# Kernel tuning notes

Measured on AMD Instinct MI355X. Metric: run time of the kernel, lower is better.

The kernel has to match this reference:

```python
import jax, jax.numpy as jnp
import numpy as np


def _quantum_act(x, act_w):
    # LearnedQuantumActivation, eval mode (no phase noise): softmax-weighted mix of 9 activations
    w = jax.nn.softmax(act_w)
    mish = x * jnp.tanh(jax.nn.softplus(x))
    return (w[0] * jax.nn.sigmoid(x) + w[1] * jax.nn.elu(x) + w[2] * jnp.tanh(x)
            + w[3] * jax.nn.relu(x) + w[4] * jax.nn.silu(x)
            + w[5] * jax.nn.gelu(x, approximate=False) + w[6] * jax.nn.selu(x)
            + w[7] * mish + w[8] * x)


def setup_inputs() -> dict:
    B, D, U, N = 1024, 1024, 2048, 4      # batch, input_dim, max_units, num_branches
    M, MD, O, H = 2048, 1024, 512, 64     # memory_size, memory_dim, output_dim, critic hidden
    key = jax.random.key(0)
    ks = jax.random.split(key, 16)
    g = lambda k, shape, s=0.02: jax.random.normal(k, shape, dtype=jnp.float32) * s
    return {
        "x": jax.random.normal(ks[0], (B, D), dtype=jnp.float32),
        "w": g(ks[1], (D, U, N)),
        "b": jnp.zeros((U, N), jnp.float32),
        "gate_w": g(ks[2], (D, N)), "gate_b": jnp.zeros((N,), jnp.float32),
        "act_w": jnp.ones((9,), jnp.float32),
        "mask": jnp.ones((U,), jnp.float32),          # neuron_mask, initial_units == max_units
        "mem": g(ks[3], (M, MD), 0.05),
        "att_w": g(ks[4], (U, M)), "att_b": jnp.zeros((M,), jnp.float32),
        "write_w": g(ks[5], (U, MD)), "write_b": jnp.zeros((MD,), jnp.float32),
        "update_gate": jnp.full((M,), 0.5, jnp.float32),
        "out_w": g(ks[6], (U, O)), "out_b": jnp.zeros((O,), jnp.float32),
        "cw1": g(ks[7], (MD, H // 2)), "cb1": jnp.zeros((H // 2,), jnp.float32),
        "cw2": g(ks[8], (O, H // 2)), "cb2": jnp.zeros((H // 2,), jnp.float32),
        "cw3": g(ks[9], (U, H // 2)), "cb3": jnp.zeros((H // 2,), jnp.float32),
        "cw4": g(ks[10], (3 * (H // 2), H)), "cb4": jnp.zeros((H,), jnp.float32),
        "cw5": g(ks[11], (H, 2)), "cb5": jnp.zeros((2,), jnp.float32),
        "meta_threshold": jnp.float32(0.5),
    }


def reference(x, w, b, gate_w, gate_b, act_w, mask, mem, att_w, att_b,
              write_w, write_b, update_gate, out_w, out_b,
              cw1, cb1, cw2, cb2, cw3, cb3, cw4, cb4, cw5, cb5, meta_threshold):
    # Dendritic plastic dense: per-branch projections mixed by a learned softmax branch gate
    pre = jnp.einsum('bi,iun->bun', x, w) + b               # (B, U, N)
    gate = jax.nn.softmax(x @ gate_w + gate_b, axis=-1)     # (B, N)
    hidden = _quantum_act(jnp.einsum('bun,bn->bu', pre, gate), act_w) * mask  # (B, U)
    # Episodic memory read + write (write is returned instead of in-place assign)
    read_att = jax.nn.softmax(hidden @ att_w + att_b, axis=-1)  # (B, M)
    read = read_att @ mem                                       # (B, MD)
    cand = jnp.tanh(hidden @ write_w + write_b)                 # (B, MD)
    u = (jnp.mean(read_att, axis=0) * update_gate)[:, None]     # (M, 1)
    new_mem = mem * (1.0 - u) + u * jnp.mean(cand, axis=0)      # (M, MD)
    # Prediction head
    preds = hidden @ out_w + out_b                              # (B, O)
    # Metacognitive critic gating
    mf = jax.nn.relu(read @ cw1 + cb1)
    pf = jax.nn.relu(preds @ cw2 + cb2)
    hf = jax.nn.relu(hidden @ cw3 + cb3)
    fused = jax.nn.relu(jnp.concatenate([mf, pf, hf], axis=-1) @ cw4 + cb4)
    outs = fused @ cw5 + cb5
    gating = jax.nn.sigmoid(outs[:, 0:1] - meta_threshold)
    return (preds * gating, new_mem)
```

## Files before the change

kernel.cpp:

```cpp
#include <hip/hip_runtime.h>
#include <hip/hip_bf16.h>
#include <math.h>

typedef __attribute__((ext_vector_type(4))) float f32x4;
typedef __attribute__((ext_vector_type(8))) short s16x8;
typedef __attribute__((ext_vector_type(4))) short s16x4;
typedef __hip_bfloat16 bf16;

#define MB (1024ull*1024ull)
#define GATE_OFF    (0ull)
#define ACTW_OFF    (16ull*1024)
#define U_OFF       (20ull*1024)
#define CMEAN_OFF   (28ull*1024)
#define PART_OFF    (64ull*1024)
#define HIDDEN_OFF  (1ull*MB)
#define RATT_OFF    (5ull*MB)
#define CAND_OFF    (9ull*MB)
#define PREDS_OFF   (11ull*MB)
#define READ_OFF    (13ull*MB)
#define XBF_OFF     (17ull*MB)
#define WT_OFF      (19ull*MB)
#define CATT_OFF    (35ull*MB)
#define MEMT_OFF    (49ull*MB)
#define READ2_OFF   WT_OFF

__device__ __forceinline__ short f2bf_s(float f) {
    bf16 h = __float2bfloat16(f);
    return *reinterpret_cast<short*>(&h);
}

__device__ __forceinline__ void async_load16(const bf16* g, short* l) {
    __builtin_amdgcn_global_load_lds((const __attribute__((address_space(1))) void*)g,
                                     (__attribute__((address_space(3))) void*)l, 16, 0, 0);
}

__device__ __forceinline__ float fast_tanh(float x) {
    float e2x = __expf(2.f * x);
    return 1.f - 2.f / (e2x + 1.f);
}

__device__ __forceinline__ float qact(float x, const float* w) {
    float ex  = __expf(x);
    float r1  = 1.f / (1.f + ex);
    float sig = 1.f - r1;
    float em1 = ex - 1.f;
    float elu = x > 0.f ? x : em1;
    float e2x = ex * ex;
    float th  = 1.f - 2.f / (e2x + 1.f);
    float rel = fmaxf(x, 0.f);
    float silu = x * sig;
    float u   = 0.7978845608028654f * (x + 0.044715f * x * x * x);
    float e2u = __expf(2.f * u);
    float gel = x * (1.f - 1.f / (e2u + 1.f));
    float sel = 1.0507009873554805f * (x > 0.f ? x : 1.6732632423543772f * em1);
    float t   = 1.f + ex;
    float t2  = t * t;
    float mish = x * (1.f - 2.f / (t2 + 1.f));
    return w[0]*sig + w[1]*elu + w[2]*th + w[3]*rel + w[4]*silu
         + w[5]*gel + w[6]*sel + w[7]*mish + w[8]*x;
}

__device__ __forceinline__ void do_transpose(const float* __restrict__ in,
                                             bf16* __restrict__ out, int R, int C,
                                             int bx, int by, int t) {
    __shared__ short tile[64][66];
    int k0 = by*64, n0 = bx*64;
    int tx = t & 63, ty = t >> 6;
    #pragma unroll
    for (int j = 0; j < 16; j++) {
        int k = ty + j*4;
        tile[tx][k] = f2bf_s(in[(size_t)(k0 + k)*C + n0 + tx]);
    }
    __syncthreads();
    int kp = t & 31, nrow = t >> 5;
    #pragma unroll
    for (int jj = 0; jj < 8; jj++) {
        int n = nrow + jj*8;
        unsigned lo = (unsigned short)tile[n][kp*2];
        unsigned hi = (unsigned short)tile[n][kp*2 + 1];
        *reinterpret_cast<unsigned*>(&out[(size_t)(n0 + n)*R + k0 + kp*2]) = lo | (hi << 16);
    }
}

__global__ __launch_bounds__(256) void k_prepass(
        const float* __restrict__ x, bf16* __restrict__ xbf,
        const float* __restrict__ gw, const float* __restrict__ gb,
        const float* __restrict__ aw_in,
        float* __restrict__ gate, float* __restrict__ actw,
        const float* __restrict__ w_, bf16* __restrict__ wT,
        const float* __restrict__ att_w, const float* __restrict__ write_w,
        const float* __restrict__ out_w, bf16* __restrict__ catT,
        const float* __restrict__ mem, bf16* __restrict__ memT) {
    int blk = blockIdx.x, t = threadIdx.x;
    if (blk < 1024) {
        int i = blk*256 + t;
        f32x4 v = ((const f32x4*)x)[i];
        s16x4 o;
        #pragma unroll
        for (int j = 0; j < 4; j++) o[j] = f2bf_s(v[j]);
        ((s16x4*)xbf)[i] = o;
        if (blk == 0 && t == 64) {
            float a[9]; float m = -1e30f;
            for (int i2 = 0; i2 < 9; i2++) { a[i2] = aw_in[i2]; m = fmaxf(m, a[i2]); }
            float ss = 0.f;
            for (int i2 = 0; i2 < 9; i2++) { a[i2] = __expf(a[i2]-m); ss += a[i2]; }
            float inv = 1.f / ss;
            for (int i2 = 0; i2 < 9; i2++) actw[i2] = a[i2]*inv;
        }
    } else if (blk < 2048) {
        int b = blk - 1024, w = t >> 6, lane = t & 63;
        __shared__ float l[4];
        float s = 0.f;
        for (int k = lane; k < 1024; k += 64)
            s += x[(size_t)b*1024 + k] * gw[k*4 + w];
        #pragma unroll
        for (int off = 32; off; off >>= 1) s += __shfl_xor(s, off);
        if (lane == 0) l[w] = s + gb[w];
        __syncthreads();
        if (t == 0) {
            float m = fmaxf(fmaxf(l[0], l[1]), fmaxf(l[2], l[3]));
            float e0 = __expf(l[0]-m), e1 = __expf(l[1]-m), e2 = __expf(l[2]-m), e3 = __expf(l[3]-m);
            float inv = 1.f / (e0+e1+e2+e3);
            gate[b*4+0] = e0*inv; gate[b*4+1] = e1*inv;
            gate[b*4+2] = e2*inv; gate[b*4+3] = e3*inv;
        }
    } else if (blk < 4096) {
        int rel = blk - 2048;
        do_transpose(w_, wT, 1024, 8192, rel & 127, rel >> 7, t);
    } else if (blk < 5120) {
        int rel = blk - 4096;
        do_transpose(att_w, catT, 2048, 2048, rel & 31, rel >> 5, t);
    } else if (blk < 5632) {
        int rel = blk - 5120;
        do_transpose(write_w, catT + 2048ull*2048, 2048, 1024, rel & 15, rel >> 4, t);
    } else if (blk < 5888) {
        int rel = blk - 5632;
        do_transpose(out_w, catT + 3072ull*2048, 2048, 512, rel & 7, rel >> 3, t);
    } else {
        int rel = blk - 5888;
        do_transpose(mem, memT, 2048, 1024, rel & 15, rel >> 4, t);
    }
}

template <int MODE, int TM>
__global__ __launch_bounds__(256, 2) void gemm_bt(
        const bf16* __restrict__ A, const bf16* __restrict__ Bt,
        int K, int lda, int ldb, int kOffset,
        const float* __restrict__ bias, const float* __restrict__ bias2,
        const float* __restrict__ bias3,
        float* __restrict__ outF, float* __restrict__ outF2,
        bf16* __restrict__ outH, bf16* __restrict__ outH2,
        const float* __restrict__ gate, const float* __restrict__ actw,
        const float* __restrict__ mask, int outStride) {
    constexpr int MI = TM / 32;
    __shared__ __align__(16) union SMem {
        struct { short a[2][TM*32]; short b[2][128*32]; } tl;
        float z[TM*32];
    } sm;
    int t = threadIdx.x, lane = t & 63;
    int rowBase = blockIdx.y * TM, colBase = blockIdx.x * 128;
    int lm = lane & 15, lq = lane >> 4;
    int w = t >> 6;
    int qm = (w >> 1) * (TM/2), qn = (w & 1) * 64;

    A  += (size_t)kOffset * blockIdx.z;
    Bt += (size_t)kOffset * blockIdx.z;

    f32x4 acc[MI][4];
    #pragma unroll
    for (int i = 0; i < MI; i++)
        #pragma unroll
        for (int j = 0; j < 4; j++) acc[i][j] = (f32x4){0.f, 0.f, 0.f, 0.f};

    int cb0 = w*128 + lane, cb1 = cb0 + 64;
    int rb0 = cb0 >> 2, kb0 = (cb0 & 3) * 8;
    int rb1 = cb1 >> 2, kb1 = (cb1 & 3) * 8;
    int ca0 = (TM == 128) ? (w*128 + lane) : (w*64 + lane);
    int ra0 = ca0 >> 2, ka0 = (ca0 & 3) * 8;
    int ra1 = (ca0 + 64) >> 2, ka1 = ((ca0 + 64) & 3) * 8;

    auto issueLoads = [&](int k0, int ib) {
        short* bA = sm.tl.a[ib];
        short* bB = sm.tl.b[ib];
        async_load16(A + (size_t)(rowBase + ra0)*lda + k0 + ka0,
                     bA + ((TM == 128) ? w*1024 : w*512));
        if (TM == 128)
            async_load16(A + (size_t)(rowBase + ra1)*lda + k0 + ka1, bA + w*1024 + 512);
        async_load16(Bt + (size_t)(colBase + rb0)*ldb + k0 + kb0, bB + w*1024);
        async_load16(Bt + (size_t)(colBase + rb1)*ldb + k0 + kb1, bB + w*1024 + 512);
    };

    issueLoads(0, 0);
    int ib = 0;
    for (int k0 = 0; k0 < K; k0 += 32) {
        __syncthreads();
        if (k0 + 32 < K) issueLoads(k0 + 32, ib ^ 1);
        const short* cA = sm.tl.a[ib];
        const short* cB = sm.tl.b[ib];
        s16x8 af[MI], bfr[4];
        #pragma unroll
        for (int mi = 0; mi < MI; mi++)
            af[mi] = *reinterpret_cast<const s16x8*>(cA + (qm + mi*16 + lm)*32 + lq*8);
        #pragma unroll
        for (int ni = 0; ni < 4; ni++)
            bfr[ni] = *reinterpret_cast<const s16x8*>(cB + (qn + ni*16 + lm)*32 + lq*8);
        #pragma unroll
        for (int mi = 0; mi < MI; mi++)
            #pragma unroll
            for (int ni = 0; ni < 4; ni++)
                acc[mi][ni] = __builtin_amdgcn_mfma_f32_16x16x32_bf16(af[mi], bfr[ni], acc[mi][ni], 0, 0, 0);
        ib ^= 1;
    }

    if (MODE == 4) {
        __syncthreads();
        #pragma unroll
        for (int mi = 0; mi < MI; mi++) {
            int rowl0 = qm + mi*16 + lq*4;
            #pragma unroll
            for (int ni = 0; ni < 4; ni++) {
                int col = colBase + qn + ni*16 + lm;
                int n = col & 3;
                float bb = bias[col];
                f32x4 v = acc[mi][ni];
                #pragma unroll
                for (int r = 0; r < 4; r++) v[r] = (v[r] + bb) * gate[(rowBase + rowl0 + r)*4 + n];
                #pragma unroll
                for (int r = 0; r < 4; r++) v[r] += __shfl_xor(v[r], 1);
                #pragma unroll
                for (int r = 0; r < 4; r++) v[r] += __shfl_xor(v[r], 2);
                if ((lane & 3) == 0) {
                    int ul = ((w & 1) << 4) + ni*4 + (lm >> 2);
                    #pragma unroll
                    for (int r = 0; r < 4; r++)
                        sm.z[(rowl0 + r)*32 + ul] = v[r];
                }
            }
        }
        __syncthreads();
        float aw[9];
        #pragma unroll
        for (int i = 0; i < 9; i++) aw[i] = actw[i];
        int u0 = colBase >> 2;
        #pragma unroll
        for (int i = 0; i < TM/8; i++) {
            int idx = t + i*256;
            int row = idx >> 5, ul = idx & 31;
            int ug = u0 + ul;
            float zz = sm.z[idx];
            outH[(size_t)(rowBase + row)*outStride + ug] = __float2bfloat16(qact(zz, aw) * mask[ug]);
        }
    } else if (MODE == 5) {
        #pragma unroll
        for (int mi = 0; mi < MI; mi++) {
            int row0 = rowBase + qm + mi*16 + lq*4;
            #pragma unroll
            for (int ni = 0; ni < 4; ni++) {
                int col = colBase + qn + ni*16 + lm;
                if (col < 2048) {
                    float bb = bias[col];
                    #pragma unroll
                    for (int r = 0; r < 4; r++)
                        outH[(size_t)(row0 + r)*2048 + col] = __float2bfloat16(acc[mi][ni][r] + bb);
                } else if (col < 3072) {
                    int c = col - 2048;
                    float bb = bias2[c];
                    #pragma unroll
                    for (int r = 0; r < 4; r++)
                        outH2[(size_t)(row0 + r)*1024 + c] = __float2bfloat16(fast_tanh(acc[mi][ni][r] + bb));
                } else {
                    int c = col - 3072;
                    float bb = bias3[c];
                    #pragma unroll
                    for (int r = 0; r < 4; r++)
                        outF[(size_t)(row0 + r)*512 + c] = acc[mi][ni][r] + bb;
                }
            }
        }
    } else {
        float* of = blockIdx.z ? outF2 : outF;
        #pragma unroll
        for (int mi = 0; mi < MI; mi++) {
            int row0 = rowBase + qm + mi*16 + lq*4;
            #pragma unroll
            for (int ni = 0; ni < 4; ni++) {
                int col = colBase + qn + ni*16 + lm;
                #pragma unroll
                for (int r = 0; r < 4; r++)
                    of[(size_t)(row0 + r)*outStride + col] = acc[mi][ni][r];
            }
        }
    }
}

__global__ __launch_bounds__(256) void k_softmax(bf16* __restrict__ ratt) {
    int b = blockIdx.x, t = threadIdx.x, w = t >> 6, lane = t & 63;
    __shared__ float red[8];
    bf16* row = ratt + (size_t)b*2048;
    float v[8];
    float mx = -1e30f;
    #pragma unroll
    for (int j = 0; j < 8; j++) {
        v[j] = __bfloat162float(row[t + j*256]);
        mx = fmaxf(mx, v[j]);
    }
    #pragma unroll
    for (int off = 32; off; off >>= 1) mx = fmaxf(mx, __shfl_xor(mx, off));
    if (lane == 0) red[w] = mx;
    __syncthreads();
    mx = fmaxf(fmaxf(red[0], red[1]), fmaxf(red[2], red[3]));
    float s = 0.f;
    #pragma unroll
    for (int j = 0; j < 8; j++) { v[j] = __expf(v[j] - mx); s += v[j]; }
    #pragma unroll
    for (int off = 32; off; off >>= 1) s += __shfl_xor(s, off);
    if (lane == 0) red[4 + w] = s;
    __syncthreads();
    float inv = 1.f / (red[4] + red[5] + red[6] + red[7]);
    #pragma unroll
    for (int j = 0; j < 8; j++)
        row[t + j*256] = __float2bfloat16(v[j] * inv);
}

__global__ __launch_bounds__(256) void k_colpart(const bf16* __restrict__ ratt,
                                                 const bf16* __restrict__ cand,
                                                 float* __restrict__ part) {
    int ct = blockIdx.x, rc = blockIdx.y, t = threadIdx.x;
    int col = ct*256 + t;
    const bf16* src; int stride, c;
    if (ct < 8) { src = ratt; stride = 2048; c = col; }
    else        { src = cand; stride = 1024; c = col - 2048; }
    float s = 0.f;
    int r0 = rc*128;
    for (int r = 0; r < 128; r++)
        s += __bfloat162float(src[(size_t)(r0 + r)*stride + c]);
    part[rc*3072 + col] = s;
}

__global__ __launch_bounds__(256) void k_colfin(const float* __restrict__ part,
                                                const float* __restrict__ update_gate,
                                                float* __restrict__ u,
                                                float* __restrict__ cmean) {
    int col = blockIdx.x*256 + threadIdx.x;
    float s = 0.f;
    #pragma unroll
    for (int rc = 0; rc < 8; rc++) s += part[rc*3072 + col];
    s *= (1.f/1024.f);
    if (col < 2048) u[col] = s * update_gate[col];
    else            cmean[col - 2048] = s;
}

__global__ __launch_bounds__(256) void k_newmem(const float* __restrict__ mem,
                                                const float* __restrict__ u,
                                                const float* __restrict__ cmean,
                                                float* __restrict__ out1) {
    int idx = blockIdx.x*256 + threadIdx.x;
    int m = idx >> 10, d = idx & 1023;
    float um = u[m];
    out1[idx] = mem[idx] * (1.f - um) + um * cmean[d];
}

__global__ __launch_bounds__(256) void k_critic(
        const float* __restrict__ readv, const float* __restrict__ readv2,
        const float* __restrict__ preds, const bf16* __restrict__ hidden,
        const float* cw1, const float* cb1, const float* cw2, const float* cb2,
        const float* cw3, const float* cb3, const float* cw4, const float* cb4,
        const float* cw5, const float* cb5, const float* thr,
        float* __restrict__ out0) {
    __shared__ __align__(16) float sx[2*1024];
    __shared__ __align__(16) float sp[2*512];
    __shared__ __align__(16) short sh[2*2048];
    __shared__ __align__(16) f32x4 part[2][32][8];
    __shared__ float feat[2][96];
    __shared__ float fused[2][64];
    __shared__ float gsh[2];
    int b0 = blockIdx.x * 2, t = threadIdx.x;
    int j4 = t & 7, kg = t >> 3;

    ((f32x4*)sx)[t]       = ((const f32x4*)(readv + (size_t)b0*1024))[t]
                          + ((const f32x4*)(readv2 + (size_t)b0*1024))[t];
    ((f32x4*)sx)[t + 256] = ((const f32x4*)(readv + (size_t)b0*1024))[t + 256]
                          + ((const f32x4*)(readv2 + (size_t)b0*1024))[t + 256];
    ((f32x4*)sp)[t]       = ((const f32x4*)(preds + (size_t)b0*512))[t];
    ((s16x8*)sh)[t]       = ((const s16x8*)(hidden + (size_t)b0*2048))[t];
    ((s16x8*)sh)[t + 256] = ((const s16x8*)(hidden + (size_t)b0*2048))[t + 256];
    __syncthreads();

    {
        const f32x4* wv = (const f32x4*)cw1;
        f32x4 a0 = (f32x4){0,0,0,0}, a1 = (f32x4){0,0,0,0};
        int k0 = kg*32;
        #pragma unroll 4
        for (int k = k0; k < k0 + 32; k++) {
            f32x4 wq = wv[k*8 + j4];
            a0 += sx[k] * wq;
            a1 += sx[1024 + k] * wq;
        }
        part[0][kg][j4] = a0; part[1][kg][j4] = a1;
    }
    __syncthreads();
    if (t < 64) {
        int r = t >> 5, f = t & 31;
        float s = 0.f;
        #pragma unroll
        for (int i = 0; i < 32; i++) s += part[r][i][f >> 2][f & 3];
        feat[r][f] = fmaxf(s + cb1[f], 0.f);
    }
    __syncthreads();
    {
        const f32x4* wv = (const f32x4*)cw2;
        f32x4 a0 = (f32x4){0,0,0,0}, a1 = (f32x4){0,0,0,0};
        int k0 = kg*16;
        #pragma unroll 4
        for (int k = k0; k < k0 + 16; k++) {
            f32x4 wq = wv[k*8 + j4];
            a0 += sp[k] * wq;
            a1 += sp[512 + k] * wq;
        }
        part[0][kg][j4] = a0; part[1][kg][j4] = a1;
    }
    __syncthreads();
    if (t < 64) {
        int r = t >> 5, f = t & 31;
        float s = 0.f;
        #pragma unroll
        for (int i = 0; i < 32; i++) s += part[r][i][f >> 2][f & 3];
        feat[r][32 + f] = fmaxf(s + cb2[f], 0.f);
    }
    __syncthreads();
    {
        const f32x4* wv = (const f32x4*)cw3;
        f32x4 a0 = (f32x4){0,0,0,0}, a1 = (f32x4){0,0,0,0};
        int k0 = kg*64;
        #pragma unroll 4
        for (int k = k0; k < k0 + 64; k++) {
            f32x4 wq = wv[k*8 + j4];
            float h0 = __bfloat162float(*reinterpret_cast<const bf16*>(&sh[k]));
            float h1 = __bfloat162float(*reinterpret_cast<const bf16*>(&sh[2048 + k]));
            a0 += h0 * wq;
            a1 += h1 * wq;
        }
        part[0][kg][j4] = a0; part[1][kg][j4] = a1;
    }
    __syncthreads();
    if (t < 64) {
        int r = t >> 5, f = t & 31;
        float s = 0.f;
        #pragma unroll
        for (int i = 0; i < 32; i++) s += part[r][i][f >> 2][f & 3];
        feat[r][64 + f] = fmaxf(s + cb3[f], 0.f);
    }
    __syncthreads();
    if (t < 128) {
        int r = t >> 6, uu = t & 63;
        float s = 0.f;
        #pragma unroll 8
        for (int k = 0; k < 96; k++) s += feat[r][k] * cw4[k*64 + uu];
        fused[r][uu] = fmaxf(s + cb4[uu], 0.f);
    }
    __syncthreads();
    if (t < 128) {
        int r = t >> 6, lane = t & 63;
        float v = fused[r][lane] * cw5[lane*2];
        #pragma unroll
        for (int off = 32; off; off >>= 1) v += __shfl_xor(v, off);
        if (lane == 0)
            gsh[r] = 1.f / (1.f + __expf(-(v + cb5[0] - thr[0])));
    }
    __syncthreads();
    #pragma unroll
    for (int idx = t; idx < 1024; idx += 256) {
        int r = idx >> 9, o = idx & 511;
        out0[(size_t)(b0 + r)*512 + o] = sp[r*512 + o] * gsh[r];
    }
}

extern "C" void kernel_launch(void* const* d_in, const int* in_sizes, int n_in,
                              void* d_out, int out_size, void* d_ws, size_t ws_size,
                              hipStream_t stream) {
    const float* x        = (const float*)d_in[0];
    const float* w_       = (const float*)d_in[1];
    const float* b_bias   = (const float*)d_in[2];
    const float* gate_w   = (const float*)d_in[3];
    const float* gate_b   = (const float*)d_in[4];
    const float* act_w    = (const float*)d_in[5];
    const float* mask     = (const float*)d_in[6];
    const float* mem      = (const float*)d_in[7];
    const float* att_w    = (const float*)d_in[8];
    const float* att_b    = (const float*)d_in[9];
    const float* write_w  = (const float*)d_in[10];
    const float* write_b  = (const float*)d_in[11];
    const float* upd_gate = (const float*)d_in[12];
    const float* out_w    = (const float*)d_in[13];
    const float* out_b    = (const float*)d_in[14];
    const float* cw1 = (const float*)d_in[15]; const float* cb1 = (const float*)d_in[16];
    const float* cw2 = (const float*)d_in[17]; const float* cb2 = (const float*)d_in[18];
    const float* cw3 = (const float*)d_in[19]; const float* cb3 = (const float*)d_in[20];
    const float* cw4 = (const float*)d_in[21]; const float* cb4 = (const float*)d_in[22];
    const float* cw5 = (const float*)d_in[23]; const float* cb5 = (const float*)d_in[24];
    const float* thr = (const float*)d_in[25];

    char* ws = (char*)d_ws;
    float* gate   = (float*)(ws + GATE_OFF);
    float* actw   = (float*)(ws + ACTW_OFF);
    float* uvec   = (float*)(ws + U_OFF);
    float* cmean  = (float*)(ws + CMEAN_OFF);
    float* part   = (float*)(ws + PART_OFF);
    bf16*  hidden = (bf16*)(ws + HIDDEN_OFF);
    bf16*  ratt   = (bf16*)(ws + RATT_OFF);
    bf16*  cand   = (bf16*)(ws + CAND_OFF);
    float* preds  = (float*)(ws + PREDS_OFF);
    float* readv  = (float*)(ws + READ_OFF);
    float* readv2 = (float*)(ws + READ2_OFF);
    bf16*  xbf    = (bf16*)(ws + XBF_OFF);
    bf16*  wT     = (bf16*)(ws + WT_OFF);
    bf16*  catT   = (bf16*)(ws + CATT_OFF);
    bf16*  memT   = (bf16*)(ws + MEMT_OFF);

    float* out0 = (float*)d_out;
    float* out1 = out0 + 1024*512;

    k_prepass<<<6400, 256, 0, stream>>>(x, xbf, gate_w, gate_b, act_w, gate, actw,
        w_, wT, att_w, write_w, out_w, catT, mem, memT);

    gemm_bt<4, 64><<<dim3(64, 16), 256, 0, stream>>>(xbf, wT, 1024, 1024, 1024, 0,
        b_bias, nullptr, nullptr, nullptr, nullptr, hidden, nullptr, gate, actw, mask, 2048);
    gemm_bt<5, 64><<<dim3(28, 16), 256, 0, stream>>>(hidden, catT, 2048, 2048, 2048, 0,
        att_b, write_b, out_b, preds, nullptr, ratt, cand, nullptr, nullptr, nullptr, 0);
    k_softmax<<<1024, 256, 0, stream>>>(ratt);
    gemm_bt<3, 64><<<dim3(8, 16, 2), 256, 0, stream>>>(ratt, memT, 1024, 2048, 2048, 1024,
        nullptr, nullptr, nullptr, readv, readv2, nullptr, nullptr, nullptr, nullptr, nullptr, 1024);

    k_colpart<<<dim3(12, 8), 256, 0, stream>>>(ratt, cand, part);
    k_colfin<<<12, 256, 0, stream>>>(part, upd_gate, uvec, cmean);
    k_newmem<<<8192, 256, 0, stream>>>(mem, uvec, cmean, out1);
    k_critic<<<512, 256, 0, stream>>>(readv, readv2, preds, hidden,
        cw1, cb1, cw2, cb2, cw3, cb3, cw4, cb4, cw5, cb5, thr, out0);
}
```

Before: 279.6 us.

## Overlap weight transposes with first GEMM and deepen split-K for memory read

Moves the att/write/out/mem weight transposes out of the prepass into the same launch as the first GEMM, so those blocks overlap with the GEMM blocks instead of running before it. The first GEMM now uses 128-row tiles, and the shared-memory union gains a transpose tile so one allocation serves both roles. The read GEMM splits K four ways instead of two, and the critic sums four partials, to raise occupancy on the small GEMM. The extra partial buffers are laid out past readv2 and the tile shape change may alter register pressure.

Measured after the change: 269.7 us. 3.5% less time.

```diff
diff --git a/kernel.cpp b/kernel.cpp
--- a/kernel.cpp
+++ b/kernel.cpp
@@ -62,22 +62,21 @@
 
 __device__ __forceinline__ void do_transpose(const float* __restrict__ in,
                                              bf16* __restrict__ out, int R, int C,
-                                             int bx, int by, int t) {
-    __shared__ short tile[64][66];
+                                             int bx, int by, int t, short* tile) {
     int k0 = by*64, n0 = bx*64;
     int tx = t & 63, ty = t >> 6;
     #pragma unroll
     for (int j = 0; j < 16; j++) {
         int k = ty + j*4;
-        tile[tx][k] = f2bf_s(in[(size_t)(k0 + k)*C + n0 + tx]);
+        tile[tx*66 + k] = f2bf_s(in[(size_t)(k0 + k)*C + n0 + tx]);
     }
     __syncthreads();
     int kp = t & 31, nrow = t >> 5;
     #pragma unroll
     for (int jj = 0; jj < 8; jj++) {
         int n = nrow + jj*8;
-        unsigned lo = (unsigned short)tile[n][kp*2];
-        unsigned hi = (unsigned short)tile[n][kp*2 + 1];
+        unsigned lo = (unsigned short)tile[n*66 + kp*2];
+        unsigned hi = (unsigned short)tile[n*66 + kp*2 + 1];
         *reinterpret_cast<unsigned*>(&out[(size_t)(n0 + n)*R + k0 + kp*2]) = lo | (hi << 16);
     }
 }
@@ -87,10 +86,8 @@
         const float* __restrict__ gw, const float* __restrict__ gb,
         const float* __restrict__ aw_in,
         float* __restrict__ gate, float* __restrict__ actw,
-        const float* __restrict__ w_, bf16* __restrict__ wT,
-        const float* __restrict__ att_w, const float* __restrict__ write_w,
-        const float* __restrict__ out_w, bf16* __restrict__ catT,
-        const float* __restrict__ mem, bf16* __restrict__ memT) {
+        const float* __restrict__ w_, bf16* __restrict__ wT) {
+    __shared__ short tile[64*66];
     int blk = blockIdx.x, t = threadIdx.x;
     if (blk < 1024) {
         int i = blk*256 + t;
@@ -124,26 +121,22 @@
             gate[b*4+0] = e0*inv; gate[b*4+1] = e1*inv;
             gate[b*4+2] = e2*inv; gate[b*4+3] = e3*inv;
         }
-    } else if (blk < 4096) {
+    } else {
         int rel = blk - 2048;
-        do_transpose(w_, wT, 1024, 8192, rel & 127, rel >> 7, t);
-    } else if (blk < 5120) {
-        int rel = blk - 4096;
-        do_transpose(att_w, catT, 2048, 2048, rel & 31, rel >> 5, t);
-    } else if (blk < 5632) {
-        int rel = blk - 5120;
-        do_transpose(write_w, catT + 2048ull*2048, 2048, 1024, rel & 15, rel >> 4, t);
-    } else if (blk < 5888) {
-        int rel = blk - 5632;
-        do_transpose(out_w, catT + 3072ull*2048, 2048, 512, rel & 7, rel >> 3, t);
-    } else {
-        int rel = blk - 5888;
-        do_transpose(mem, memT, 2048, 1024, rel & 15, rel >> 4, t);
-    }
-}
+        do_transpose(w_, wT, 1024, 8192, rel & 127, rel >> 7, t, tile);
+    }
+}
+
+template <int TM>
+union SMemT {
+    struct { short a[2][TM*32]; short b[2][128*32]; } tl;
+    float z[TM*32];
+    short tr[64*66];
+};
 
 template <int MODE, int TM>
-__global__ __launch_bounds__(256, 2) void gemm_bt(
+__device__ __forceinline__ void gemm_core(
+        int bx, int by, int bz, SMemT<TM>& sm,
         const bf16* __restrict__ A, const bf16* __restrict__ Bt,
         int K, int lda, int ldb, int kOffset,
         const float* __restrict__ bias, const float* __restrict__ bias2,
@@ -153,18 +146,14 @@
         const float* __restrict__ gate, const float* __restrict__ actw,
         const float* __restrict__ mask, int outStride) {
     constexpr int MI = TM / 32;
-    __shared__ __align__(16) union SMem {
-        struct { short a[2][TM*32]; short b[2][128*32]; } tl;
-        float z[TM*32];
-    } sm;
     int t = threadIdx.x, lane = t & 63;
-    int rowBase = blockIdx.y * TM, colBase = blockIdx.x * 128;
+    int rowBase = by * TM, colBase = bx * 128;
     int lm = lane & 15, lq = lane >> 4;
     int w = t >> 6;
     int qm = (w >> 1) * (TM/2), qn = (w & 1) * 64;
 
-    A  += (size_t)kOffset * blockIdx.z;
-    Bt += (size_t)kOffset * blockIdx.z;
+    A  += (size_t)kOffset * bz;
+    Bt += (size_t)kOffset * bz;
 
     f32x4 acc[MI][4];
     #pragma unroll
@@ -278,7 +267,7 @@
             }
         }
     } else {
-        float* of = blockIdx.z ? outF2 : outF;
+        float* of = bz ? (outF2 + (size_t)(bz - 1) * 1048576) : outF;
         #pragma unroll
         for (int mi = 0; mi < MI; mi++) {
             int row0 = rowBase + qm + mi*16 + lq*4;
@@ -289,6 +278,53 @@
                 for (int r = 0; r < 4; r++)
                     of[(size_t)(row0 + r)*outStride + col] = acc[mi][ni][r];
             }
+        }
+    }
+}
+
+template <int MODE, int TM>
+__global__ __launch_bounds__(256, 2) void gemm_bt(
+        const bf16* __restrict__ A, const bf16* __restrict__ Bt,
+        int K, int lda, int ldb, int kOffset,
+        const float* __restrict__ bias, const float* __restrict__ bias2,
+        const float* __restrict__ bias3,
+        float* __restrict__ outF, float* __restrict__ outF2,
+        bf16* __restrict__ outH, bf16* __restrict__ outH2,
+        const float* __restrict__ gate, const float* __restrict__ actw,
+        const float* __restrict__ mask, int outStride) {
+    __shared__ __align__(16) SMemT<TM> sm;
+    gemm_core<MODE, TM>(blockIdx.x, blockIdx.y, blockIdx.z, sm,
+                        A, Bt, K, lda, ldb, kOffset, bias, bias2, bias3,
+                        outF, outF2, outH, outH2, gate, actw, mask, outStride);
+}
+
+__global__ __launch_bounds__(256, 2) void k_g1x(
+        const bf16* __restrict__ xbf, const bf16* __restrict__ wT,
+        const float* __restrict__ bias, bf16* __restrict__ hidden,
+        const float* __restrict__ gate, const float* __restrict__ actw,
+        const float* __restrict__ mask,
+        const float* __restrict__ att_w, const float* __restrict__ write_w,
+        const float* __restrict__ out_w, bf16* __restrict__ catT,
+        const float* __restrict__ mem, bf16* __restrict__ memT) {
+    __shared__ __align__(16) SMemT<128> sm;
+    int bid = blockIdx.x, t = threadIdx.x;
+    if (bid < 512) {
+        gemm_core<4, 128>(bid & 63, bid >> 6, 0, sm, xbf, wT, 1024, 1024, 1024, 0,
+                          bias, nullptr, nullptr, nullptr, nullptr, hidden, nullptr,
+                          gate, actw, mask, 2048);
+    } else {
+        int rel = bid - 512;
+        if (rel < 1024) {
+            do_transpose(att_w, catT, 2048, 2048, rel & 31, rel >> 5, t, sm.tr);
+        } else if (rel < 1536) {
+            rel -= 1024;
+            do_transpose(write_w, catT + 2048ull*2048, 2048, 1024, rel & 15, rel >> 4, t, sm.tr);
+        } else if (rel < 1792) {
+            rel -= 1536;
+            do_transpose(out_w, catT + 3072ull*2048, 2048, 512, rel & 7, rel >> 3, t, sm.tr);
+        } else {
+            rel -= 1792;
+            do_transpose(mem, memT, 2048, 1024, rel & 15, rel >> 4, t, sm.tr);
         }
     }
 }
@@ -377,10 +413,14 @@
     int b0 = blockIdx.x * 2, t = threadIdx.x;
     int j4 = t & 7, kg = t >> 3;
 
-    ((f32x4*)sx)[t]       = ((const f32x4*)(readv + (size_t)b0*1024))[t]
-                          + ((const f32x4*)(readv2 + (size_t)b0*1024))[t];
-    ((f32x4*)sx)[t + 256] = ((const f32x4*)(readv + (size_t)b0*1024))[t + 256]
-                          + ((const f32x4*)(readv2 + (size_t)b0*1024))[t + 256];
+    {
+        const f32x4* r0 = (const f32x4*)(readv  + (size_t)b0*1024);
+        const f32x4* r1 = (const f32x4*)(readv2 + (size_t)b0*1024);
+        const f32x4* r2 = (const f32x4*)(readv2 + 1048576 + (size_t)b0*1024);
+        const f32x4* r3 = (const f32x4*)(readv2 + 2097152 + (size_t)b0*1024);
+        ((f32x4*)sx)[t]       = r0[t] + r1[t] + r2[t] + r3[t];
+        ((f32x4*)sx)[t + 256] = r0[t + 256] + r1[t + 256] + r2[t + 256] + r3[t + 256];
+    }
     ((f32x4*)sp)[t]       = ((const f32x4*)(preds + (size_t)b0*512))[t];
     ((s16x8*)sh)[t]       = ((const s16x8*)(hidden + (size_t)b0*2048))[t];
     ((s16x8*)sh)[t + 256] = ((const s16x8*)(hidden + (size_t)b0*2048))[t + 256];
@@ -520,15 +560,15 @@
     float* out0 = (float*)d_out;
     float* out1 = out0 + 1024*512;
 
-    k_prepass<<<6400, 256, 0, stream>>>(x, xbf, gate_w, gate_b, act_w, gate, actw,
-        w_, wT, att_w, write_w, out_w, catT, mem, memT);
-
-    gemm_bt<4, 64><<<dim3(64, 16), 256, 0, stream>>>(xbf, wT, 1024, 1024, 1024, 0,
-        b_bias, nullptr, nullptr, nullptr, nullptr, hidden, nullptr, gate, actw, mask, 2048);
+    k_prepass<<<4096, 256, 0, stream>>>(x, xbf, gate_w, gate_b, act_w, gate, actw, w_, wT);
+
+    k_g1x<<<2816, 256, 0, stream>>>(xbf, wT, b_bias, hidden, gate, actw, mask,
+                                    att_w, write_w, out_w, catT, mem, memT);
+
     gemm_bt<5, 64><<<dim3(28, 16), 256, 0, stream>>>(hidden, catT, 2048, 2048, 2048, 0,
         att_b, write_b, out_b, preds, nullptr, ratt, cand, nullptr, nullptr, nullptr, 0);
     k_softmax<<<1024, 256, 0, stream>>>(ratt);
-    gemm_bt<3, 64><<<dim3(8, 16, 2), 256, 0, stream>>>(ratt, memT, 1024, 2048, 2048, 1024,
+    gemm_bt<3, 64><<<dim3(8, 16, 4), 256, 0, stream>>>(ratt, memT, 512, 2048, 2048, 512,
         nullptr, nullptr, nullptr, readv, readv2, nullptr, nullptr, nullptr, nullptr, nullptr, 1024);
 
     k_colpart<<<dim3(12, 8), 256, 0, stream>>>(ratt, cand, part);
```
